# Kernel tuning notes

Measured on AMD Instinct MI355X. Metric: run time of the kernel, lower is better.

Reference implementation:

```python
import jax, jax.numpy as jnp
import numpy as np

B, N = 8, 2048
DIN, DH, DE = 32, 64, 64
R = 3          # number_relations
L = 3          # num_layers -> 1 first + 1 block + 1 last
PRED_IN = DH * (L - 1) + DE  # concat: 64*2 + 64 = 192
EPS_BN = 1e-5
EPS_NORM = 1e-12


def setup_inputs() -> dict:
    key = jax.random.key(0)
    ks = jax.random.split(key, 12)
    x = jax.random.normal(ks[0], (B, N, DIN), jnp.float32)
    # relation labels in {0..R}; 0 = no edge, 1..R = relation type
    relation = jax.random.randint(ks[1], (B, N, N), 0, R + 1).astype(jnp.int32)
    # adjacency is the 0/1 edge indicator (float), as the torch code treats it
    adj = (relation > 0).astype(jnp.float32)
    s = 0.05
    w_first = jax.random.normal(ks[2], (R, DIN, DH), jnp.float32) * s
    b_first = jnp.zeros((DH,), jnp.float32)
    w_block = jax.random.normal(ks[3], (R, DH, DH), jnp.float32) * s
    b_block = jnp.zeros((DH,), jnp.float32)
    w_last = jax.random.normal(ks[4], (R, DH, DE), jnp.float32) * s
    b_last = jnp.zeros((DE,), jnp.float32)
    w_map = jax.random.normal(ks[5], (PRED_IN, DE), jnp.float32) * s
    b_map = jnp.zeros((DE,), jnp.float32)
    return {"x": x, "relation": relation, "adj": adj,
            "w_first": w_first, "b_first": b_first,
            "w_block": w_block, "b_block": b_block,
            "w_last": w_last, "b_last": b_last,
            "w_map": w_map, "b_map": b_map}


def _graph_conv(x, rel, W, b):
    # rel: [B,N,N] (int labels or float adjacency); W: [R, din, dout]
    y = jnp.zeros((x.shape[0], x.shape[1], W.shape[2]), x.dtype)
    for i in range(R):  # fixed, small relation count
        mask = (rel == (i + 1)).astype(x.dtype)            # [B,N,N]
        h = jnp.einsum('bij,bjd->bid', mask, x)            # masked aggregation
        y = y + jnp.einsum('bid,de->bie', h, W[i])
    y = y + b
    # F.normalize(p=2, dim=2): v / max(||v||, eps)
    nrm = jnp.sqrt(jnp.sum(y * y, axis=2, keepdims=True))
    return y / jnp.maximum(nrm, EPS_NORM)


def _apply_bn(x):
    # fresh BatchNorm1d(N) in training mode, affine weight=1/bias=0:
    # normalize over (batch, feature) per node index, biased variance
    mean = jnp.mean(x, axis=(0, 2), keepdims=True)
    var = jnp.mean(jnp.square(x - mean), axis=(0, 2), keepdims=True)
    return (x - mean) * jax.lax.rsqrt(var + EPS_BN)


def reference(x, relation, adj, w_first, b_first, w_block, b_block,
              w_last, b_last, w_map, b_map):
    # conv_first uses `relation`
    h = _apply_bn(jax.nn.relu(_graph_conv(x, relation, w_first, b_first)))
    out_all = [jnp.max(h, axis=1)]
    # conv_block and conv_last are (faithfully) called with `adj` as relation
    h = _apply_bn(jax.nn.relu(_graph_conv(h, adj, w_block, b_block)))
    out_all.append(jnp.max(h, axis=1))
    h = _graph_conv(h, adj, w_last, b_last)
    out_all.append(jnp.max(h, axis=1))
    output = jnp.concatenate(out_all, axis=1)        # [B, PRED_IN]
    ypred = output @ w_map + b_map                   # map_model Linear
    return (output, ypred)
```

## Files before the change

kernel.cpp:

```cpp
#include <hip/hip_runtime.h>


#define NN 2048

typedef short short8 __attribute__((ext_vector_type(8)));
typedef float floatx4 __attribute__((ext_vector_type(4)));

__device__ __forceinline__ unsigned short f2bf(float x) {
  unsigned u = __float_as_uint(x);
  u += 0x7FFFu + ((u >> 16) & 1u);
  return (unsigned short)(u >> 16);
}

__device__ __forceinline__ int kvirt(int k) {
  const int chunk = k >> 10, kin = k & 1023;
  return chunk * 1024 + ((kin >> 2) & 63) * 16 + ((kin >> 8) & 3) * 4 +
         (kin & 3);
}

__global__ __launch_bounds__(256) void k_xw1(const float* __restrict__ x,
                                             const float* __restrict__ w,
                                             unsigned short* __restrict__ xws,
                                             unsigned* __restrict__ done) {
  __shared__ __align__(16) char smemc[16640];
  const int u = blockIdx.x, tid = threadIdx.x;
  if (u == 0 && tid == 0) *done = 0u;
  float* xs = (float*)smemc;
  float* wsh = (float*)(smemc + 64 * 33 * 4);
  const int jc = u & 31, b = (u >> 5) & 7, r = u >> 8;
  const int j0 = jc * 64;
  for (int idx = tid; idx < 64 * 32; idx += 256) {
    int row = idx >> 5, f = idx & 31;
    xs[row * 33 + f] = x[((long)b * NN + j0 + row) * 32 + f];
    wsh[idx] = w[r * 2048 + idx];
  }
  __syncthreads();
  const int j = tid & 63, g = tid >> 6;
  const int V = kvirt(j0 + j);
  const int kblk = V >> 5, kq = (V >> 3) & 3, kj = V & 7;
  unsigned short* dst =
      xws + (((long)(r * 8 + b) * 64 + kblk) * 4 + g) * 512 + kj;
  float xr[32];
#pragma unroll
  for (int f = 0; f < 32; ++f) xr[f] = xs[j * 33 + f];
#pragma unroll
  for (int ii = 0; ii < 16; ++ii) {
    float acc = 0.f;
#pragma unroll
    for (int f = 0; f < 32; ++f) acc += xr[f] * wsh[f * 64 + g * 16 + ii];
    dst[(kq * 16 + ii) * 8] = f2bf(acc);
  }
}

template <bool RELU, bool POOL3>
__device__ __forceinline__ void gemm_epilogue(
    char* smem, int b, int it, int tid, floatx4 (&acc)[4][4],
    const float* __restrict__ bias, float* __restrict__ Hout,
    float* __restrict__ part3) {
  floatx4* cb = (floatx4*)smem;
  const int wave = tid >> 6, lane = tid & 63;
  const int m = lane & 15, kq = lane >> 4;
  const int i0 = it * 64;
  if (wave >= 4) {
    const int src = wave - 4;
#pragma unroll
    for (int rs = 0; rs < 4; ++rs)
#pragma unroll
      for (int t = 0; t < 4; ++t)
        cb[((rs * 4 + src) * 4 + t) * 64 + lane] = acc[rs][t];
  }
  __syncthreads();
  if (wave < 4) {
#pragma unroll
    for (int rs = 0; rs < 4; ++rs)
#pragma unroll
      for (int t = 0; t < 4; ++t) {
        const int ix = ((rs * 4 + wave) * 4 + t) * 64 + lane;
        cb[ix] = cb[ix] + acc[rs][t];
      }
  }
  __syncthreads();
  if (wave < 4) {
    const int rs = wave;
    floatx4 s[4];
#pragma unroll
    for (int t = 0; t < 4; ++t) s[t] = cb[((rs * 4 + 0) * 4 + t) * 64 + lane];
#pragma unroll
    for (int src = 1; src < 4; ++src)
#pragma unroll
      for (int t = 0; t < 4; ++t)
        s[t] += cb[((rs * 4 + src) * 4 + t) * 64 + lane];
    float bv[4];
#pragma unroll
    for (int t = 0; t < 4; ++t) bv[t] = bias[t * 16 + m];
    float pmt[4] = {-3.4e38f, -3.4e38f, -3.4e38f, -3.4e38f};
#pragma unroll
    for (int reg = 0; reg < 4; ++reg) {
#pragma unroll
      for (int t = 0; t < 4; ++t) s[t][reg] += bv[t];
      float q = s[0][reg] * s[0][reg] + s[1][reg] * s[1][reg] +
                s[2][reg] * s[2][reg] + s[3][reg] * s[3][reg];
#pragma unroll
      for (int off = 1; off <= 8; off <<= 1) q += __shfl_xor(q, off);
      q = 1.0f / fmaxf(sqrtf(q), 1e-12f);
#pragma unroll
      for (int t = 0; t < 4; ++t) {
        float o = s[t][reg] * q;
        if (RELU) o = fmaxf(o, 0.0f);
        if (POOL3)
          pmt[t] = fmaxf(pmt[t], o);
        else
          Hout[((long)b * NN + i0 + rs * 16 + kq * 4 + reg) * 64 + t * 16 +
               m] = o;
      }
    }
    if (POOL3) {
#pragma unroll
      for (int t = 0; t < 4; ++t) {
        pmt[t] = fmaxf(pmt[t], __shfl_xor(pmt[t], 16));
        pmt[t] = fmaxf(pmt[t], __shfl_xor(pmt[t], 32));
      }
      float* pm = (float*)(smem + wave * 16384);
      if (kq == 0) {
#pragma unroll
        for (int t = 0; t < 4; ++t) pm[t * 16 + m] = pmt[t];
      }
    }
  }
}

template <int NREL>
__device__ __forceinline__ void gemm_chunk_mfma(
    const unsigned* mw, const uint2* lut, const unsigned short* __restrict__ xws,
    int b, int chunk, int wave, int lane, floatx4 (&acc)[4][4]) {
  const int m = lane & 15, kq = lane >> 4;
  const unsigned shamt = kq * 8;
#pragma unroll
  for (int j = 0; j < 4; ++j) {
    const int kk = j * 8 + wave;
    const int kblk = chunk * 32 + kk;
#pragma unroll
    for (int p = 0; p < NREL; ++p) {
      const unsigned short* bb =
          xws + ((long)(p * 8 + b) * 64 + kblk) * 2048 + lane * 8;
      short8 bf0 = *(const short8*)(bb);
      short8 bf1 = *(const short8*)(bb + 512);
      short8 bf2 = *(const short8*)(bb + 1024);
      short8 bf3 = *(const short8*)(bb + 1536);
#pragma unroll
      for (int rs = 0; rs < 4; ++rs) {
        unsigned word = mw[(p * 64 + rs * 16 + m) * 33 + kk];
        unsigned byte = (word >> shamt) & 0xffu;
        uint2 lo = lut[byte & 15u];
        uint2 hi = lut[byte >> 4];
        union {
          unsigned uu[4];
          short8 s8;
        } fr;
        fr.uu[0] = lo.x;
        fr.uu[1] = lo.y;
        fr.uu[2] = hi.x;
        fr.uu[3] = hi.y;
        acc[rs][0] = __builtin_amdgcn_mfma_f32_16x16x32_bf16(fr.s8, bf0,
                                                             acc[rs][0], 0, 0, 0);
        acc[rs][1] = __builtin_amdgcn_mfma_f32_16x16x32_bf16(fr.s8, bf1,
                                                             acc[rs][1], 0, 0, 0);
        acc[rs][2] = __builtin_amdgcn_mfma_f32_16x16x32_bf16(fr.s8, bf2,
                                                             acc[rs][2], 0, 0, 0);
        acc[rs][3] = __builtin_amdgcn_mfma_f32_16x16x32_bf16(fr.s8, bf3,
                                                             acc[rs][3], 0, 0, 0);
      }
    }
  }
}

__global__ __launch_bounds__(512) void k_gemm_rel(
    const int* __restrict__ rel, const unsigned short* __restrict__ xws,
    const float* __restrict__ bias, float* __restrict__ Hout,
    unsigned* __restrict__ pu) {
  __shared__ __align__(16) char smem[65536];
  unsigned* mw = (unsigned*)smem;
  uint2* lut = (uint2*)(smem + 3 * 8448);
  const int bid = blockIdx.x;
  const int b = bid & 7, it = bid >> 3;
  const int tid = threadIdx.x;
  const int wave = tid >> 6, lane = tid & 63;
  const int i0 = it * 64;

  if (tid < 16) {
    unsigned n = tid;
    lut[n] =
        make_uint2(((n & 1u) ? 0x3f80u : 0u) | ((n & 2u) ? 0x3f800000u : 0u),
                   ((n & 4u) ? 0x3f80u : 0u) | ((n & 8u) ? 0x3f800000u : 0u));
  }

  floatx4 acc[4][4];
#pragma unroll
  for (int rs = 0; rs < 4; ++rs)
#pragma unroll
    for (int t = 0; t < 4; ++t) acc[rs][t] = floatx4{0, 0, 0, 0};

  unsigned short* mh = (unsigned short*)mw;
  unsigned short* puh = (unsigned short*)pu;
  const long rowbase = (long)b * NN + i0;

  for (int chunk = 0; chunk < 2; ++chunk) {
    int4 v[4];
    {
      const int4* rp =
          (const int4*)(rel + (rowbase + wave * 8) * NN + chunk * 1024);
#pragma unroll
      for (int c = 0; c < 4; ++c) v[c] = rp[c * 64 + lane];
    }
#pragma unroll
    for (int rr = 0; rr < 8; ++rr) {
      const int row = wave * 8 + rr;
      int4 vn[4];
      if (rr < 7) {
        const int4* rp =
            (const int4*)(rel + (rowbase + row + 1) * NN + chunk * 1024);
#pragma unroll
        for (int c = 0; c < 4; ++c) vn[c] = rp[c * 64 + lane];
      }
      unsigned m0 = 0, m1 = 0, m2 = 0;
#pragma unroll
      for (int c = 0; c < 4; ++c) {
        int vv[4] = {v[c].x, v[c].y, v[c].z, v[c].w};
#pragma unroll
        for (int j = 0; j < 4; ++j) {
          unsigned bit = 1u << (c * 4 + j);
          m0 |= (vv[j] == 1) ? bit : 0u;
          m1 |= (vv[j] == 2) ? bit : 0u;
          m2 |= (vv[j] == 3) ? bit : 0u;
        }
      }
      const int hw = (row * 33 + (lane >> 1)) * 2 + (lane & 1);
      mh[hw] = (unsigned short)m0;
      mh[4224 + hw] = (unsigned short)m1;
      mh[8448 + hw] = (unsigned short)m2;
      puh[((rowbase + row) * 64 + chunk * 32) * 2 + lane] =
          (unsigned short)(m0 | m1 | m2);
#pragma unroll
      for (int c = 0; c < 4; ++c) v[c] = vn[c];
    }
    __syncthreads();
    gemm_chunk_mfma<3>(mw, lut, xws, b, chunk, wave, lane, acc);
    __syncthreads();
  }
  gemm_epilogue<true, false>(smem, b, it, tid, acc, bias, Hout, nullptr);
}

template <bool RELU, bool POOL3>
__global__ __launch_bounds__(512) void k_gemm_u(
    const unsigned* __restrict__ pu, const unsigned short* __restrict__ xws,
    const float* __restrict__ bias, float* __restrict__ Hout,
    float* __restrict__ part3, const float* __restrict__ PP1,
    const float* __restrict__ PP2, float* __restrict__ out,
    const float* __restrict__ wmap, const float* __restrict__ bmap,
    unsigned* __restrict__ done) {
  __shared__ __align__(16) char smem[65536];
  __shared__ int s_last;
  unsigned* mw = (unsigned*)smem;
  uint2* lut = (uint2*)(smem + 8448);
  const int bid = blockIdx.x;
  const int b = bid & 7, it = bid >> 3;
  const int tid = threadIdx.x;
  const int wave = tid >> 6, lane = tid & 63;
  const int i0 = it * 64;

  if (tid < 16) {
    unsigned n = tid;
    lut[n] =
        make_uint2(((n & 1u) ? 0x3f80u : 0u) | ((n & 2u) ? 0x3f800000u : 0u),
                   ((n & 4u) ? 0x3f80u : 0u) | ((n & 8u) ? 0x3f800000u : 0u));
  }

  floatx4 acc[4][4];
#pragma unroll
  for (int rs = 0; rs < 4; ++rs)
#pragma unroll
    for (int t = 0; t < 4; ++t) acc[rs][t] = floatx4{0, 0, 0, 0};

  for (int chunk = 0; chunk < 2; ++chunk) {
    for (int idx = tid; idx < 2048; idx += 512) {
      int row = idx >> 5, w = idx & 31;
      mw[row * 33 + w] = pu[((long)b * NN + i0 + row) * 64 + chunk * 32 + w];
    }
    __syncthreads();
    gemm_chunk_mfma<1>(mw, lut, xws, b, chunk, wave, lane, acc);
    __syncthreads();
  }
  gemm_epilogue<RELU, POOL3>(smem, b, it, tid, acc, bias, Hout, part3);

  if (POOL3) {
    __syncthreads();
    if (tid < 64) {
      float v = -3.4e38f;
#pragma unroll
      for (int w = 0; w < 4; ++w)
        v = fmaxf(v, ((const float*)(smem + w * 16384))[tid]);
      part3[((long)b * 32 + it) * 64 + tid] = v;
    }
    __threadfence();
    __syncthreads();
    if (tid == 0) s_last = (atomicAdd(done, 1u) == 255u) ? 1 : 0;
    __syncthreads();
    if (s_last) {
      __threadfence();
      float* obuf = (float*)smem;
      const int col = tid;
      const int bb = col >> 6, e = col & 63;
      float m1 = -3.4e38f, m2 = -3.4e38f, m3 = -3.4e38f;
#pragma unroll
      for (int c = 0; c < 32; ++c) {
        m1 = fmaxf(m1, PP1[(long)c * 512 + col]);
        m2 = fmaxf(m2, PP2[(long)c * 512 + col]);
        m3 = fmaxf(m3, part3[((long)bb * 32 + c) * 64 + e]);
      }
      out[bb * 192 + e] = m1;
      out[bb * 192 + 64 + e] = m2;
      out[bb * 192 + 128 + e] = m3;
      obuf[bb * 192 + e] = m1;
      obuf[bb * 192 + 64 + e] = m2;
      obuf[bb * 192 + 128 + e] = m3;
      __syncthreads();
      float a = bmap[e];
#pragma unroll 4
      for (int k = 0; k < 192; ++k) a += obuf[bb * 192 + k] * wmap[k * 64 + e];
      out[1536 + bb * 64 + e] = a;
    }
  }
}

__global__ __launch_bounds__(256) void k_xwh_bn(const float* __restrict__ H,
                                                const float* __restrict__ w,
                                                unsigned short* __restrict__ xws,
                                                float* __restrict__ PP) {
  __shared__ float hs[64 * 65];
  __shared__ float wsh[64 * 64];
  __shared__ float sm[64], srs[64];
  const int bid = blockIdx.x, tid = threadIdx.x;
  const int jc = bid & 31, b = bid >> 5;
  const int j0 = jc * 64;
  {
    const int n = tid >> 2, q = tid & 3;
    float s1 = 0.f, s2 = 0.f;
#pragma unroll
    for (int bb = 0; bb < 8; ++bb) {
      const float4* hp =
          (const float4*)(H + ((long)bb * NN + j0 + n) * 64 + q * 16);
#pragma unroll
      for (int c = 0; c < 4; ++c) {
        float4 v = hp[c];
        s1 += v.x + v.y + v.z + v.w;
        s2 += v.x * v.x + v.y * v.y + v.z * v.z + v.w * v.w;
      }
    }
    s1 += __shfl_xor(s1, 1);
    s2 += __shfl_xor(s2, 1);
    s1 += __shfl_xor(s1, 2);
    s2 += __shfl_xor(s2, 2);
    if (q == 0) {
      float mean = s1 * (1.0f / 512.0f);
      float var = fmaxf(s2 * (1.0f / 512.0f) - mean * mean, 0.0f);
      sm[n] = mean;
      srs[n] = rsqrtf(var + 1e-5f);
    }
  }
  __syncthreads();
  for (int idx = tid; idx < 4096; idx += 256) {
    int row = idx >> 6, f = idx & 63;
    float v = H[((long)b * NN + j0 + row) * 64 + f];
    hs[row * 65 + f] = (v - sm[row]) * srs[row];
    wsh[idx] = w[idx];
  }
  __syncthreads();
  {
    const int j = tid & 63, g = tid >> 6;
    const int V = kvirt(j0 + j);
    const int kblk = V >> 5, kq = (V >> 3) & 3, kj = V & 7;
    unsigned short* dst = xws + (((long)b * 64 + kblk) * 4 + g) * 512 + kj;
    float acc[16];
#pragma unroll
    for (int ii = 0; ii < 16; ++ii) acc[ii] = 0.f;
#pragma unroll
    for (int c = 0; c < 4; ++c) {
      float xr[16];
#pragma unroll
      for (int f = 0; f < 16; ++f) xr[f] = hs[j * 65 + c * 16 + f];
#pragma unroll
      for (int ii = 0; ii < 16; ++ii)
#pragma unroll
        for (int f = 0; f < 16; ++f)
          acc[ii] += xr[f] * wsh[(c * 16 + f) * 64 + g * 16 + ii];
    }
#pragma unroll
    for (int ii = 0; ii < 16; ++ii) dst[(kq * 16 + ii) * 8] = f2bf(acc[ii]);
  }
  if (b == 0) {
#pragma unroll
    for (int part = 0; part < 2; ++part) {
      const int col = part * 256 + tid;
      const int bb = col >> 6, e = col & 63;
      float mx = -3.4e38f;
      for (int n = 0; n < 64; ++n) {
        float v = H[((long)bb * NN + j0 + n) * 64 + e];
        mx = fmaxf(mx, (v - sm[n]) * srs[n]);
      }
      PP[(long)jc * 512 + col] = mx;
    }
  }
}

extern "C" void kernel_launch(void* const* d_in, const int* in_sizes, int n_in,
                              void* d_out, int out_size, void* d_ws,
                              size_t ws_size, hipStream_t stream) {
  const float* x = (const float*)d_in[0];
  const int* rel = (const int*)d_in[1];
  const float* w_first = (const float*)d_in[3];
  const float* b_first = (const float*)d_in[4];
  const float* w_block = (const float*)d_in[5];
  const float* b_block = (const float*)d_in[6];
  const float* w_last = (const float*)d_in[7];
  const float* b_last = (const float*)d_in[8];
  const float* w_map = (const float*)d_in[9];
  const float* b_map = (const float*)d_in[10];
  float* out = (float*)d_out;

  char* ws = (char*)d_ws;
  const size_t MB = 1024 * 1024;
  unsigned* PLANES_U = (unsigned*)(ws);
  unsigned short* XWS = (unsigned short*)(ws + 4 * MB);
  float* H = (float*)(ws + 10 * MB);
  float* PP1 = (float*)(ws + 14 * MB);
  float* PP2 = (float*)(ws + 15 * MB);
  float* PART3 = (float*)(ws + 16 * MB);
  unsigned* DONE = (unsigned*)(ws + 17 * MB);

  k_xw1<<<768, 256, 0, stream>>>(x, w_first, XWS, DONE);
  k_gemm_rel<<<256, 512, 0, stream>>>(rel, XWS, b_first, H, PLANES_U);
  k_xwh_bn<<<256, 256, 0, stream>>>(H, w_block, XWS, PP1);
  k_gemm_u<true, false><<<256, 512, 0, stream>>>(
      PLANES_U, XWS, b_block, H, nullptr, nullptr, nullptr, nullptr, nullptr,
      nullptr, nullptr);
  k_xwh_bn<<<256, 256, 0, stream>>>(H, w_last, XWS, PP2);
  k_gemm_u<false, true><<<256, 512, 0, stream>>>(
      PLANES_U, XWS, b_last, nullptr, PART3, PP1, PP2, out, w_map, b_map,
      DONE);
}
```

Before: 392.2 us.

## Fuse GEMM and batchnorm stages into one cooperative persistent kernel with grid barriers

Merges the five kernels that ran after the first projection into a single cooperative kernel of 256 blocks × 512 threads. Stages are separated by atomic-counter grid barriers, and block 0 computes the final pooling and map step at the end. The batchnorm/XW kernel is reworked for 512 threads so it matches the fused block size. The aim is to remove kernel launch gaps and per-launch overhead, at the cost of spin-wait barrier latency and a persistent-grid occupancy constraint.

```diff
diff --git a/kernel.cpp b/kernel.cpp
--- a/kernel.cpp
+++ b/kernel.cpp
@@ -18,13 +18,27 @@
          (kin & 3);
 }
 
+__device__ __forceinline__ void gbar(unsigned* ctr, int tid) {
+  __syncthreads();
+  if (tid == 0) {
+    __threadfence();
+    __hip_atomic_fetch_add(ctr, 1u, __ATOMIC_ACQ_REL,
+                           __HIP_MEMORY_SCOPE_AGENT);
+    while (__hip_atomic_load(ctr, __ATOMIC_RELAXED,
+                             __HIP_MEMORY_SCOPE_AGENT) < 256u)
+      __builtin_amdgcn_s_sleep(1);
+    __threadfence();
+  }
+  __syncthreads();
+}
+
 __global__ __launch_bounds__(256) void k_xw1(const float* __restrict__ x,
                                              const float* __restrict__ w,
                                              unsigned short* __restrict__ xws,
-                                             unsigned* __restrict__ done) {
+                                             unsigned* __restrict__ ctrs) {
   __shared__ __align__(16) char smemc[16640];
   const int u = blockIdx.x, tid = threadIdx.x;
-  if (u == 0 && tid == 0) *done = 0u;
+  if (u == 0 && tid < 128) ctrs[tid] = 0u;
   float* xs = (float*)smemc;
   float* wsh = (float*)(smemc + 64 * 33 * 4);
   const int jc = u & 31, b = (u >> 5) & 7, r = u >> 8;
@@ -55,8 +69,7 @@
 template <bool RELU, bool POOL3>
 __device__ __forceinline__ void gemm_epilogue(
     char* smem, int b, int it, int tid, floatx4 (&acc)[4][4],
-    const float* __restrict__ bias, float* __restrict__ Hout,
-    float* __restrict__ part3) {
+    const float* __restrict__ bias, float* __restrict__ Hout) {
   floatx4* cb = (floatx4*)smem;
   const int wave = tid >> 6, lane = tid & 63;
   const int m = lane & 15, kq = lane >> 4;
@@ -131,8 +144,9 @@
 
 template <int NREL>
 __device__ __forceinline__ void gemm_chunk_mfma(
-    const unsigned* mw, const uint2* lut, const unsigned short* __restrict__ xws,
-    int b, int chunk, int wave, int lane, floatx4 (&acc)[4][4]) {
+    const unsigned* mw, const uint2* lut,
+    const unsigned short* __restrict__ xws, int b, int chunk, int wave,
+    int lane, floatx4 (&acc)[4][4]) {
   const int m = lane & 15, kq = lane >> 4;
   const unsigned shamt = kq * 8;
 #pragma unroll
@@ -174,16 +188,15 @@
   }
 }
 
-__global__ __launch_bounds__(512) void k_gemm_rel(
-    const int* __restrict__ rel, const unsigned short* __restrict__ xws,
-    const float* __restrict__ bias, float* __restrict__ Hout,
-    unsigned* __restrict__ pu) {
-  __shared__ __align__(16) char smem[65536];
+__device__ void dev_gemm_rel(char* smem, int bid, int tid,
+                             const int* __restrict__ rel,
+                             const unsigned short* __restrict__ xws,
+                             const float* __restrict__ bias,
+                             float* __restrict__ Hout,
+                             unsigned* __restrict__ pu) {
   unsigned* mw = (unsigned*)smem;
   uint2* lut = (uint2*)(smem + 3 * 8448);
-  const int bid = blockIdx.x;
   const int b = bid & 7, it = bid >> 3;
-  const int tid = threadIdx.x;
   const int wave = tid >> 6, lane = tid & 63;
   const int i0 = it * 64;
 
@@ -247,24 +260,19 @@
     gemm_chunk_mfma<3>(mw, lut, xws, b, chunk, wave, lane, acc);
     __syncthreads();
   }
-  gemm_epilogue<true, false>(smem, b, it, tid, acc, bias, Hout, nullptr);
+  gemm_epilogue<true, false>(smem, b, it, tid, acc, bias, Hout);
 }
 
 template <bool RELU, bool POOL3>
-__global__ __launch_bounds__(512) void k_gemm_u(
-    const unsigned* __restrict__ pu, const unsigned short* __restrict__ xws,
-    const float* __restrict__ bias, float* __restrict__ Hout,
-    float* __restrict__ part3, const float* __restrict__ PP1,
-    const float* __restrict__ PP2, float* __restrict__ out,
-    const float* __restrict__ wmap, const float* __restrict__ bmap,
-    unsigned* __restrict__ done) {
-  __shared__ __align__(16) char smem[65536];
-  __shared__ int s_last;
+__device__ void dev_gemm_u(char* smem, int bid, int tid,
+                           const unsigned* __restrict__ pu,
+                           const unsigned short* __restrict__ xws,
+                           const float* __restrict__ bias,
+                           float* __restrict__ Hout,
+                           float* __restrict__ part3) {
   unsigned* mw = (unsigned*)smem;
   uint2* lut = (uint2*)(smem + 8448);
-  const int bid = blockIdx.x;
   const int b = bid & 7, it = bid >> 3;
-  const int tid = threadIdx.x;
   const int wave = tid >> 6, lane = tid & 63;
   const int i0 = it * 64;
 
@@ -290,7 +298,7 @@
     gemm_chunk_mfma<1>(mw, lut, xws, b, chunk, wave, lane, acc);
     __syncthreads();
   }
-  gemm_epilogue<RELU, POOL3>(smem, b, it, tid, acc, bias, Hout, part3);
+  gemm_epilogue<RELU, POOL3>(smem, b, it, tid, acc, bias, Hout);
 
   if (POOL3) {
     __syncthreads();
@@ -301,56 +309,29 @@
         v = fmaxf(v, ((const float*)(smem + w * 16384))[tid]);
       part3[((long)b * 32 + it) * 64 + tid] = v;
     }
-    __threadfence();
-    __syncthreads();
-    if (tid == 0) s_last = (atomicAdd(done, 1u) == 255u) ? 1 : 0;
-    __syncthreads();
-    if (s_last) {
-      __threadfence();
-      float* obuf = (float*)smem;
-      const int col = tid;
-      const int bb = col >> 6, e = col & 63;
-      float m1 = -3.4e38f, m2 = -3.4e38f, m3 = -3.4e38f;
-#pragma unroll
-      for (int c = 0; c < 32; ++c) {
-        m1 = fmaxf(m1, PP1[(long)c * 512 + col]);
-        m2 = fmaxf(m2, PP2[(long)c * 512 + col]);
-        m3 = fmaxf(m3, part3[((long)bb * 32 + c) * 64 + e]);
-      }
-      out[bb * 192 + e] = m1;
-      out[bb * 192 + 64 + e] = m2;
-      out[bb * 192 + 128 + e] = m3;
-      obuf[bb * 192 + e] = m1;
-      obuf[bb * 192 + 64 + e] = m2;
-      obuf[bb * 192 + 128 + e] = m3;
-      __syncthreads();
-      float a = bmap[e];
-#pragma unroll 4
-      for (int k = 0; k < 192; ++k) a += obuf[bb * 192 + k] * wmap[k * 64 + e];
-      out[1536 + bb * 64 + e] = a;
-    }
-  }
-}
-
-__global__ __launch_bounds__(256) void k_xwh_bn(const float* __restrict__ H,
-                                                const float* __restrict__ w,
-                                                unsigned short* __restrict__ xws,
-                                                float* __restrict__ PP) {
-  __shared__ float hs[64 * 65];
-  __shared__ float wsh[64 * 64];
-  __shared__ float sm[64], srs[64];
-  const int bid = blockIdx.x, tid = threadIdx.x;
+  }
+}
+
+__device__ void dev_xwh_bn512(char* smemc, int bid, int tid,
+                              const float* __restrict__ H,
+                              const float* __restrict__ w,
+                              unsigned short* __restrict__ xws,
+                              float* __restrict__ PP) {
+  float* hs = (float*)smemc;
+  float* wsh = (float*)(smemc + 16640);
+  float* sm = (float*)(smemc + 16640 + 16384);
+  float* srs = (float*)(smemc + 16640 + 16384 + 256);
   const int jc = bid & 31, b = bid >> 5;
   const int j0 = jc * 64;
   {
-    const int n = tid >> 2, q = tid & 3;
+    const int n = tid >> 3, o = tid & 7;
     float s1 = 0.f, s2 = 0.f;
 #pragma unroll
     for (int bb = 0; bb < 8; ++bb) {
       const float4* hp =
-          (const float4*)(H + ((long)bb * NN + j0 + n) * 64 + q * 16);
-#pragma unroll
-      for (int c = 0; c < 4; ++c) {
+          (const float4*)(H + ((long)bb * NN + j0 + n) * 64 + o * 8);
+#pragma unroll
+      for (int c = 0; c < 2; ++c) {
         float4 v = hp[c];
         s1 += v.x + v.y + v.z + v.w;
         s2 += v.x * v.x + v.y * v.y + v.z * v.z + v.w * v.w;
@@ -360,7 +341,9 @@
     s2 += __shfl_xor(s2, 1);
     s1 += __shfl_xor(s1, 2);
     s2 += __shfl_xor(s2, 2);
-    if (q == 0) {
+    s1 += __shfl_xor(s1, 4);
+    s2 += __shfl_xor(s2, 4);
+    if (o == 0) {
       float mean = s1 * (1.0f / 512.0f);
       float var = fmaxf(s2 * (1.0f / 512.0f) - mean * mean, 0.0f);
       sm[n] = mean;
@@ -368,7 +351,7 @@
     }
   }
   __syncthreads();
-  for (int idx = tid; idx < 4096; idx += 256) {
+  for (int idx = tid; idx < 4096; idx += 512) {
     int row = idx >> 6, f = idx & 63;
     float v = H[((long)b * NN + j0 + row) * 64 + f];
     hs[row * 65 + f] = (v - sm[row]) * srs[row];
@@ -376,40 +359,93 @@
   }
   __syncthreads();
   {
-    const int j = tid & 63, g = tid >> 6;
+    const int j = tid & 63, gg = tid >> 6;
+    const int g = gg & 3, hf = gg >> 2;
     const int V = kvirt(j0 + j);
     const int kblk = V >> 5, kq = (V >> 3) & 3, kj = V & 7;
     unsigned short* dst = xws + (((long)b * 64 + kblk) * 4 + g) * 512 + kj;
-    float acc[16];
-#pragma unroll
-    for (int ii = 0; ii < 16; ++ii) acc[ii] = 0.f;
+    float acc[8];
+#pragma unroll
+    for (int ii = 0; ii < 8; ++ii) acc[ii] = 0.f;
 #pragma unroll
     for (int c = 0; c < 4; ++c) {
       float xr[16];
 #pragma unroll
       for (int f = 0; f < 16; ++f) xr[f] = hs[j * 65 + c * 16 + f];
 #pragma unroll
-      for (int ii = 0; ii < 16; ++ii)
+      for (int ii = 0; ii < 8; ++ii)
 #pragma unroll
         for (int f = 0; f < 16; ++f)
-          acc[ii] += xr[f] * wsh[(c * 16 + f) * 64 + g * 16 + ii];
-    }
-#pragma unroll
-    for (int ii = 0; ii < 16; ++ii) dst[(kq * 16 + ii) * 8] = f2bf(acc[ii]);
+          acc[ii] += xr[f] * wsh[(c * 16 + f) * 64 + g * 16 + hf * 8 + ii];
+    }
+#pragma unroll
+    for (int ii = 0; ii < 8; ++ii)
+      dst[(kq * 16 + hf * 8 + ii) * 8] = f2bf(acc[ii]);
   }
   if (b == 0) {
-#pragma unroll
-    for (int part = 0; part < 2; ++part) {
-      const int col = part * 256 + tid;
-      const int bb = col >> 6, e = col & 63;
-      float mx = -3.4e38f;
-      for (int n = 0; n < 64; ++n) {
-        float v = H[((long)bb * NN + j0 + n) * 64 + e];
-        mx = fmaxf(mx, (v - sm[n]) * srs[n]);
-      }
-      PP[(long)jc * 512 + col] = mx;
-    }
-  }
+    const int col = tid;
+    const int bb = col >> 6, e = col & 63;
+    float mx = -3.4e38f;
+    for (int n = 0; n < 64; ++n) {
+      float v = H[((long)bb * NN + j0 + n) * 64 + e];
+      mx = fmaxf(mx, (v - sm[n]) * srs[n]);
+    }
+    PP[(long)jc * 512 + col] = mx;
+  }
+}
+
+__device__ void dev_tail(char* smemc, int tid, const float* __restrict__ PP1,
+                         const float* __restrict__ PP2,
+                         const float* __restrict__ P3, float* __restrict__ out,
+                         const float* __restrict__ wmap,
+                         const float* __restrict__ bmap) {
+  float* obuf = (float*)smemc;
+  const int col = tid;
+  const int bb = col >> 6, e = col & 63;
+  float m1 = -3.4e38f, m2 = -3.4e38f, m3 = -3.4e38f;
+#pragma unroll
+  for (int c = 0; c < 32; ++c) {
+    m1 = fmaxf(m1, PP1[(long)c * 512 + col]);
+    m2 = fmaxf(m2, PP2[(long)c * 512 + col]);
+    m3 = fmaxf(m3, P3[((long)bb * 32 + c) * 64 + e]);
+  }
+  out[bb * 192 + e] = m1;
+  out[bb * 192 + 64 + e] = m2;
+  out[bb * 192 + 128 + e] = m3;
+  obuf[bb * 192 + e] = m1;
+  obuf[bb * 192 + 64 + e] = m2;
+  obuf[bb * 192 + 128 + e] = m3;
+  __syncthreads();
+  float acc = bmap[e];
+#pragma unroll 4
+  for (int k = 0; k < 192; ++k) acc += obuf[bb * 192 + k] * wmap[k * 64 + e];
+  out[1536 + bb * 64 + e] = acc;
+}
+
+__global__ __launch_bounds__(512) void k_mega(
+    const int* __restrict__ rel, const unsigned short* __restrict__ xws_c,
+    unsigned short* __restrict__ xws, const float* __restrict__ b_first,
+    const float* __restrict__ w_block, const float* __restrict__ b_block,
+    const float* __restrict__ w_last, const float* __restrict__ b_last,
+    const float* __restrict__ wmap, const float* __restrict__ bmap,
+    unsigned* __restrict__ pu, float* __restrict__ H,
+    float* __restrict__ PP1, float* __restrict__ PP2,
+    float* __restrict__ PART3, float* __restrict__ out,
+    unsigned* __restrict__ ctrs) {
+  __shared__ __align__(16) char smem[65536];
+  const int bid = blockIdx.x, tid = threadIdx.x;
+
+  dev_gemm_rel(smem, bid, tid, rel, xws_c, b_first, H, pu);
+  gbar(&ctrs[0], tid);
+  dev_xwh_bn512(smem, bid, tid, H, w_block, xws, PP1);
+  gbar(&ctrs[16], tid);
+  dev_gemm_u<true, false>(smem, bid, tid, pu, xws_c, b_block, H, nullptr);
+  gbar(&ctrs[32], tid);
+  dev_xwh_bn512(smem, bid, tid, H, w_last, xws, PP2);
+  gbar(&ctrs[48], tid);
+  dev_gemm_u<false, true>(smem, bid, tid, pu, xws_c, b_last, nullptr, PART3);
+  gbar(&ctrs[64], tid);
+  if (bid == 0) dev_tail(smem, tid, PP1, PP2, PART3, out, wmap, bmap);
 }
 
 extern "C" void kernel_launch(void* const* d_in, const int* in_sizes, int n_in,
@@ -429,22 +465,19 @@
 
   char* ws = (char*)d_ws;
   const size_t MB = 1024 * 1024;
-  unsigned* PLANES_U = (unsigned*)(ws);
+  unsigned* PU = (unsigned*)(ws);
   unsigned short* XWS = (unsigned short*)(ws + 4 * MB);
   float* H = (float*)(ws + 10 * MB);
   float* PP1 = (float*)(ws + 14 * MB);
   float* PP2 = (float*)(ws + 15 * MB);
   float* PART3 = (float*)(ws + 16 * MB);
-  unsigned* DONE = (unsigned*)(ws + 17 * MB);
-
-  k_xw1<<<768, 256, 0, stream>>>(x, w_first, XWS, DONE);
-  k_gemm_rel<<<256, 512, 0, stream>>>(rel, XWS, b_first, H, PLANES_U);
-  k_xwh_bn<<<256, 256, 0, stream>>>(H, w_block, XWS, PP1);
-  k_gemm_u<true, false><<<256, 512, 0, stream>>>(
-      PLANES_U, XWS, b_block, H, nullptr, nullptr, nullptr, nullptr, nullptr,
-      nullptr, nullptr);
-  k_xwh_bn<<<256, 256, 0, stream>>>(H, w_last, XWS, PP2);
-  k_gemm_u<false, true><<<256, 512, 0, stream>>>(
-      PLANES_U, XWS, b_last, nullptr, PART3, PP1, PP2, out, w_map, b_map,
-      DONE);
-}
+  unsigned* CTRS = (unsigned*)(ws + 17 * MB);
+
+  k_xw1<<<768, 256, 0, stream>>>(x, w_first, XWS, CTRS);
+  const unsigned short* XWS_C = XWS;
+  void* kargs[] = {&rel,  &XWS_C,  &XWS,   &b_first, &w_block, &b_block,
+                   &w_last, &b_last, &w_map, &b_map,   &PU,      &H,
+                   &PP1,    &PP2,    &PART3, &out,     &CTRS};
+  hipLaunchCooperativeKernel((void*)k_mega, dim3(256), dim3(512), kargs, 0,
+                             stream);
+}
```

Measured after the change: 481.7 us. 1.23x slower.
